# Kernel tuning notes

Measured on AMD Instinct MI355X. Metric: run time of the kernel, lower is better.

## Reference

```python
import jax, jax.numpy as jnp
import numpy as np

NUM_HEADS = 16
HEAD_DIM = 80  # head_dim_ori; NPU pads 80->128 with zeros (math-neutral)


def _rotate_half(x):
    x1, x2 = jnp.split(x, 2, axis=-1)
    return jnp.concatenate([-x2, x1], axis=-1)


def setup_inputs() -> dict:
    key = jax.random.key(0)
    ks = jax.random.split(key, 7)
    S, E = 4096, 1280
    inv = jnp.asarray(1.0 / np.sqrt(E), jnp.float32)
    # rotary tables: proper cos/sin from angles for realism
    pos = jnp.arange(S, dtype=jnp.float32)[:, None]
    freqs = 1.0 / (10000.0 ** (jnp.arange(0, HEAD_DIM // 2, dtype=jnp.float32) / (HEAD_DIM // 2)))
    ang = pos * freqs[None, :]                      # [S, 40]
    ang = jnp.concatenate([ang, ang], axis=-1)      # [S, 80] rotate-half layout
    return {
        'hidden_states': jax.random.normal(ks[0], (S, E), jnp.float32),
        'cos': jnp.cos(ang),
        'sin': jnp.sin(ang),
        'w_qkv': jax.random.normal(ks[1], (3 * E, E), jnp.float32) * inv,
        'b_qkv': jax.random.normal(ks[2], (3 * E,), jnp.float32) * 0.02,
        'w_proj': jax.random.normal(ks[3], (E, E), jnp.float32) * inv,
        'b_proj': jax.random.normal(ks[4], (E,), jnp.float32) * 0.02,
    }


def reference(hidden_states, cos, sin, w_qkv, b_qkv, w_proj, b_proj):
    S, E = hidden_states.shape
    H, D = NUM_HEADS, HEAD_DIM
    # fused QKV linear (transposeB=True, hasBias=True) then split into 3
    qkv = hidden_states @ w_qkv.T + b_qkv          # [S, 3E]
    q, k, v = jnp.split(qkv, 3, axis=-1)
    q = q.reshape(S, H, D)
    k = k.reshape(S, H, D)
    v = v.reshape(S, H, D)
    # rotate-half RoPE (rotaryCoeff=2) on q and k
    c = cos[:, None, :]
    s = sin[:, None, :]
    q = q * c + _rotate_half(q) * s
    k = k * c + _rotate_half(k) * s
    # full bidirectional self-attention (PA_ENCODER), qkScale = 1/sqrt(head_dim_ori)
    scale = jnp.asarray(1.0 / np.sqrt(D), q.dtype)
    scores = jnp.einsum('shd,thd->hst', q, k) * scale   # [H, S, S]
    attn = jax.nn.softmax(scores, axis=-1)
    out = jnp.einsum('hst,thd->shd', attn, v).reshape(S, E)
    # output projection + residual add (atten_res_add)
    dense = out @ w_proj.T + b_proj
    return hidden_states + dense
```

## Files before the change

### kernel.cpp

```cpp
#include <hip/hip_runtime.h>
#include <hip/hip_bf16.h>


#define S_LEN 4096
#define E_DIM 1280
#define NH 16
#define HD 80
#define HDP 96

typedef __bf16 bf16x8 __attribute__((ext_vector_type(8)));
typedef float f32x4 __attribute__((ext_vector_type(4)));

__device__ __forceinline__ short f2bf(float x) {
    __hip_bfloat16 h = __float2bfloat16(x);
    return __builtin_bit_cast(short, h);
}
__device__ __forceinline__ float bf2f(short x) {
    return __bfloat162float(__builtin_bit_cast(__hip_bfloat16, x));
}
__device__ __forceinline__ bf16x8 ldb(const short* p) {
    return *reinterpret_cast<const bf16x8*>(p);
}
__device__ __forceinline__ unsigned cvt_pk_bf16(float a, float b) {
    unsigned r;
    asm("v_cvt_pk_bf16_f32 %0, %1, %2" : "=v"(r) : "v"(a), "v"(b));
    return r;
}
__device__ __forceinline__ void gload16(const void* g, void* l) {
    __builtin_amdgcn_global_load_lds(
        (const __attribute__((address_space(1))) unsigned int*)g,
        (__attribute__((address_space(3))) unsigned int*)l, 16, 0, 0);
}

__global__ __launch_bounds__(256) void cast3_k(const float* __restrict__ a, short* __restrict__ oa, int na4,
                                               const float* __restrict__ b, short* __restrict__ ob, int nb4,
                                               const float* __restrict__ c, short* __restrict__ oc, int nc4) {
    int j = blockIdx.x * 256 + threadIdx.x;
    const float* src;
    short* dst;
    if (j < na4) {
        src = a; dst = oa;
    } else {
        j -= na4;
        if (j < nb4) {
            src = b; dst = ob;
        } else {
            j -= nb4;
            if (j >= nc4) return;
            src = c; dst = oc;
        }
    }
    float4 v = *reinterpret_cast<const float4*>(&src[j * 4]);
    ushort4 o;
    o.x = (unsigned short)f2bf(v.x);
    o.y = (unsigned short)f2bf(v.y);
    o.z = (unsigned short)f2bf(v.z);
    o.w = (unsigned short)f2bf(v.w);
    *reinterpret_cast<ushort4*>(&dst[j * 4]) = o;
}

__global__ __launch_bounds__(512, 2) void gemm1_256_k(
    const short* __restrict__ A, const short* __restrict__ B, const float* __restrict__ bias,
    short* __restrict__ Qraw, short* __restrict__ Kraw, short* __restrict__ Vg) {
    const int K = E_DIM;
    __shared__ short As[2][2][8192];
    __shared__ short Bs[2][2][8192];
    int t = threadIdx.x;
    int lane = t & 63, w = t >> 6;
    int wr = w >> 2, wc = w & 3;
    int lr = lane & 15, lg = lane >> 4;
    int bid = blockIdx.x;
    int swz = (bid & 7) * 30 + (bid >> 3);
    int bm = swz / 15, bn = swz % 15;
    int mb = bm * 256, nb = bn * 256;

    int lgs = (t & 3) ^ ((t >> 3) & 3);
    const short* aS = A + (size_t)(mb + (t >> 2)) * K + lgs * 8;
    const short* bS = B + (size_t)(nb + (t >> 2)) * K + lgs * 8;
    const int rowStep = 128 * K;

    int aoff[2][4], boff[4];
#pragma unroll
    for (int mq = 0; mq < 2; mq++)
#pragma unroll
        for (int ii = 0; ii < 4; ii++) {
            int r = wr * 128 + mq * 64 + ii * 16 + lr;
            aoff[mq][ii] = r * 32 + ((lg ^ ((r >> 1) & 3)) * 8);
        }
#pragma unroll
    for (int n = 0; n < 4; n++) {
        int r = wc * 64 + n * 16 + lr;
        boff[n] = r * 32 + ((lg ^ ((r >> 1) & 3)) * 8);
    }

    f32x4 acc[8][4];
#pragma unroll
    for (int i = 0; i < 8; i++)
#pragma unroll
        for (int n = 0; n < 4; n++) acc[i][n] = (f32x4){0.f, 0.f, 0.f, 0.f};

#define STG_A(d, kh, kb2)                                              \
    {                                                                  \
        gload16(aS + (kb2) + (kh)*32, &As[d][kh][w * 512]);            \
        gload16(aS + rowStep + (kb2) + (kh)*32, &As[d][kh][4096 + w * 512]); \
    }
#define STG_B(d, kh, kb2)                                              \
    {                                                                  \
        gload16(bS + (kb2) + (kh)*32, &Bs[d][kh][w * 512]);            \
        gload16(bS + rowStep + (kb2) + (kh)*32, &Bs[d][kh][4096 + w * 512]); \
    }

    STG_A(0, 0, 0);
    STG_B(0, 0, 0);
    STG_A(0, 1, 0);
    STG_B(0, 1, 0);
    asm volatile("s_waitcnt vmcnt(4)" ::: "memory");
    __builtin_amdgcn_s_barrier();
    asm volatile("" ::: "memory");

    for (int kb = 0; kb < K; kb += 64) {
        int d = (kb >> 6) & 1;
        int kb2 = kb + 64;
        bool more = kb2 < K;
        bf16x8 af[4], bfr[4];

#pragma unroll
        for (int n = 0; n < 4; n++) bfr[n] = ldb(&Bs[d][0][boff[n]]);
#pragma unroll
        for (int ii = 0; ii < 4; ii++) af[ii] = ldb(&As[d][0][aoff[0][ii]]);
        if (more) STG_A(d ^ 1, 0, kb2);
        __builtin_amdgcn_s_barrier();
        asm volatile("s_waitcnt lgkmcnt(0)" ::: "memory");
        __builtin_amdgcn_sched_barrier(0);
        __builtin_amdgcn_s_setprio(1);
#pragma unroll
        for (int ii = 0; ii < 4; ii++)
#pragma unroll
            for (int n = 0; n < 4; n++)
                acc[ii][n] = __builtin_amdgcn_mfma_f32_16x16x32_bf16(af[ii], bfr[n], acc[ii][n], 0, 0, 0);
        __builtin_amdgcn_s_setprio(0);
        __builtin_amdgcn_s_barrier();
        asm volatile("" ::: "memory");

#pragma unroll
        for (int ii = 0; ii < 4; ii++) af[ii] = ldb(&As[d][0][aoff[1][ii]]);
        if (more) {
            STG_B(d ^ 1, 0, kb2);
            asm volatile("s_waitcnt vmcnt(4)" ::: "memory");
        } else {
            asm volatile("s_waitcnt vmcnt(0)" ::: "memory");
        }
        __builtin_amdgcn_s_barrier();
        asm volatile("s_waitcnt lgkmcnt(0)" ::: "memory");
        __builtin_amdgcn_sched_barrier(0);
        __builtin_amdgcn_s_setprio(1);
#pragma unroll
        for (int ii = 0; ii < 4; ii++)
#pragma unroll
            for (int n = 0; n < 4; n++)
                acc[4 + ii][n] = __builtin_amdgcn_mfma_f32_16x16x32_bf16(af[ii], bfr[n], acc[4 + ii][n], 0, 0, 0);
        __builtin_amdgcn_s_setprio(0);
        __builtin_amdgcn_s_barrier();
        asm volatile("" ::: "memory");

#pragma unroll
        for (int n = 0; n < 4; n++) bfr[n] = ldb(&Bs[d][1][boff[n]]);
#pragma unroll
        for (int ii = 0; ii < 4; ii++) af[ii] = ldb(&As[d][1][aoff[0][ii]]);
        if (more) STG_A(d ^ 1, 1, kb2);
        __builtin_amdgcn_s_barrier();
        asm volatile("s_waitcnt lgkmcnt(0)" ::: "memory");
        __builtin_amdgcn_sched_barrier(0);
        __builtin_amdgcn_s_setprio(1);
#pragma unroll
        for (int ii = 0; ii < 4; ii++)
#pragma unroll
            for (int n = 0; n < 4; n++)
                acc[ii][n] = __builtin_amdgcn_mfma_f32_16x16x32_bf16(af[ii], bfr[n], acc[ii][n], 0, 0, 0);
        __builtin_amdgcn_s_setprio(0);
        __builtin_amdgcn_s_barrier();
        asm volatile("" ::: "memory");

#pragma unroll
        for (int ii = 0; ii < 4; ii++) af[ii] = ldb(&As[d][1][aoff[1][ii]]);
        if (more) {
            STG_B(d ^ 1, 1, kb2);
            asm volatile("s_waitcnt vmcnt(4)" ::: "memory");
        }
        __builtin_amdgcn_s_barrier();
        asm volatile("s_waitcnt lgkmcnt(0)" ::: "memory");
        __builtin_amdgcn_sched_barrier(0);
        __builtin_amdgcn_s_setprio(1);
#pragma unroll
        for (int ii = 0; ii < 4; ii++)
#pragma unroll
            for (int n = 0; n < 4; n++)
                acc[4 + ii][n] = __builtin_amdgcn_mfma_f32_16x16x32_bf16(af[ii], bfr[n], acc[4 + ii][n], 0, 0, 0);
        __builtin_amdgcn_s_setprio(0);
        __builtin_amdgcn_s_barrier();
        asm volatile("" ::: "memory");
    }
#undef STG_A
#undef STG_B

    int part = nb / E_DIM;
    short* dst = (part == 0) ? Qraw : (part == 1) ? Kraw : Vg;
    int nloc = nb - part * E_DIM;
#pragma unroll
    for (int j = 0; j < 4; j++) {
        int cn = wc * 64 + j * 16 + lr;
        float bv = bias[nb + cn];
        int col = nloc + cn;
#pragma unroll
        for (int i = 0; i < 8; i++) {
#pragma unroll
            for (int r = 0; r < 4; r++) {
                int s = mb + wr * 128 + (i >> 2) * 64 + (i & 3) * 16 + lg * 4 + r;
                dst[(size_t)s * E_DIM + col] = f2bf(acc[i][j][r] + bv);
            }
        }
    }
}

__global__ __launch_bounds__(256) void gemm_bt_k(
    const short* __restrict__ A, const short* __restrict__ B, const float* __restrict__ bias,
    const float* __restrict__ resid, float* __restrict__ Out) {
    const int K = E_DIM;
    __shared__ short As[2][128 * 64];
    __shared__ short Bs[2][128 * 64];
    int t = threadIdx.x;
    int lane = t & 63, w = t >> 6;
    int wr = w >> 1, wc = w & 1;
    int lr = lane & 15, lg = lane >> 4;
    int mb = blockIdx.y * 128, nb = blockIdx.x * 128;

    const short* asrc[4];
    const short* bsrc[4];
#pragma unroll
    for (int c = 0; c < 4; c++) {
        int p = c * 256 + t;
        int m = p >> 3;
        int kg = (p & 7) ^ (m & 7);
        asrc[c] = A + (size_t)(mb + m) * K + kg * 8;
        bsrc[c] = B + (size_t)(nb + m) * K + kg * 8;
    }
    int xa = lr & 7;
    int cx0 = ((0 * 4 + lg) ^ xa) * 8;
    int cx1 = ((1 * 4 + lg) ^ xa) * 8;
    int rowA[4], rowB[4];
#pragma unroll
    for (int i = 0; i < 4; i++) {
        rowA[i] = (wr * 64 + i * 16 + lr) * 64;
        rowB[i] = (wc * 64 + i * 16 + lr) * 64;
    }

    f32x4 acc[4][4];
#pragma unroll
    for (int i = 0; i < 4; i++)
#pragma unroll
        for (int j = 0; j < 4; j++) acc[i][j] = (f32x4){0.f, 0.f, 0.f, 0.f};

#define G_STAGE(buf, kb)                                             \
    {                                                                \
        _Pragma("unroll") for (int c = 0; c < 4; c++) {              \
            int ldso = c * 2048 + w * 512;                           \
            gload16(asrc[c] + (kb), &As[buf][ldso]);                 \
            gload16(bsrc[c] + (kb), &Bs[buf][ldso]);                 \
        }                                                            \
    }

    G_STAGE(0, 0);
    asm volatile("s_waitcnt vmcnt(0)" ::: "memory");
    __syncthreads();

    int buf = 0;
    for (int kb = 0; kb < K; kb += 64) {
        if (kb + 64 < K) G_STAGE(buf ^ 1, kb + 64);
        __builtin_amdgcn_s_setprio(1);
#pragma unroll
        for (int kk = 0; kk < 2; kk++) {
            int cx = kk ? cx1 : cx0;
            bf16x8 af[4], bfr[4];
#pragma unroll
            for (int i = 0; i < 4; i++) {
                af[i] = ldb(&As[buf][rowA[i] + cx]);
                bfr[i] = ldb(&Bs[buf][rowB[i] + cx]);
            }
#pragma unroll
            for (int i = 0; i < 4; i++)
#pragma unroll
                for (int j = 0; j < 4; j++)
                    acc[i][j] = __builtin_amdgcn_mfma_f32_16x16x32_bf16(af[i], bfr[j], acc[i][j], 0, 0, 0);
        }
        __builtin_amdgcn_s_setprio(0);
        __syncthreads();
        buf ^= 1;
    }
#undef G_STAGE

#pragma unroll
    for (int j = 0; j < 4; j++) {
        int n = nb + wc * 64 + j * 16 + lr;
        float bv = bias[n];
#pragma unroll
        for (int i = 0; i < 4; i++) {
#pragma unroll
            for (int r = 0; r < 4; r++) {
                int s = mb + wr * 64 + i * 16 + lg * 4 + r;
                Out[s * E_DIM + n] = acc[i][j][r] + bv + resid[s * E_DIM + n];
            }
        }
    }
}

__global__ __launch_bounds__(256) void rope_k(const short* __restrict__ Qraw,
                                              const short* __restrict__ Kraw,
                                              const float* __restrict__ cosp,
                                              const float* __restrict__ sinp,
                                              short* __restrict__ Qg, short* __restrict__ Kg) {
    int idx = blockIdx.x * 256 + threadIdx.x;
    int c = idx % 12;
    int hh = (idx / 12) & 15;
    int s = idx / 192;
    int base96 = ((hh * S_LEN + s)) * HDP + c * 8;
    if (c >= 10) {
        int4 z = {0, 0, 0, 0};
        *reinterpret_cast<int4*>(&Qg[base96]) = z;
        *reinterpret_cast<int4*>(&Kg[base96]) = z;
        return;
    }
    int d0 = c * 8;
    int dp = (d0 < 40) ? d0 + 40 : d0 - 40;
    float sgn = (d0 < 40) ? -1.f : 1.f;
    int base80 = s * E_DIM + hh * HD;
    float q[8], qp[8], k[8], kp[8], cs[8], sn[8];
    {
        int4 v;
        v = *reinterpret_cast<const int4*>(&Qraw[base80 + d0]);
        const short* sp = reinterpret_cast<const short*>(&v);
        for (int i = 0; i < 8; i++) q[i] = bf2f(sp[i]);
        v = *reinterpret_cast<const int4*>(&Qraw[base80 + dp]);
        for (int i = 0; i < 8; i++) qp[i] = bf2f(sp[i]);
        v = *reinterpret_cast<const int4*>(&Kraw[base80 + d0]);
        for (int i = 0; i < 8; i++) k[i] = bf2f(sp[i]);
        v = *reinterpret_cast<const int4*>(&Kraw[base80 + dp]);
        for (int i = 0; i < 8; i++) kp[i] = bf2f(sp[i]);
    }
    *reinterpret_cast<float4*>(&cs[0]) = *reinterpret_cast<const float4*>(&cosp[s * HD + d0]);
    *reinterpret_cast<float4*>(&cs[4]) = *reinterpret_cast<const float4*>(&cosp[s * HD + d0 + 4]);
    *reinterpret_cast<float4*>(&sn[0]) = *reinterpret_cast<const float4*>(&sinp[s * HD + d0]);
    *reinterpret_cast<float4*>(&sn[4]) = *reinterpret_cast<const float4*>(&sinp[s * HD + d0 + 4]);
    const float qscale = 0.16129849190f;
    short oq[8], ok[8];
#pragma unroll
    for (int i = 0; i < 8; i++) {
        oq[i] = f2bf((q[i] * cs[i] + sgn * qp[i] * sn[i]) * qscale);
        ok[i] = f2bf(k[i] * cs[i] + sgn * kp[i] * sn[i]);
    }
    *reinterpret_cast<int4*>(&Qg[base96]) = *reinterpret_cast<int4*>(oq);
    *reinterpret_cast<int4*>(&Kg[base96]) = *reinterpret_cast<int4*>(ok);
}

__global__ __launch_bounds__(256) void transpose_v_k(const short* __restrict__ Vg,
                                                     short* __restrict__ Vt) {
    __shared__ short tile[32][33];
    int h = blockIdx.z, sb = blockIdx.x * 32, db = blockIdx.y * 32;
    int t = threadIdx.x;
    for (int e = t; e < 1024; e += 256) {
        int si = e >> 5, dj = e & 31;
        int d = db + dj;
        tile[si][dj] = (d < HD) ? Vg[(size_t)(sb + si) * E_DIM + h * HD + d] : (short)0;
    }
    __syncthreads();
    for (int e = t; e < 1024; e += 256) {
        int di = e >> 5, sj = e & 31;
        int d = db + di;
        int pj = ((sj >> 2) & 3) * 8 + ((sj >> 4) & 1) * 4 + (sj & 3);
        if (d < HD) Vt[(h * HD + d) * S_LEN + sb + pj] = tile[sj][di];
    }
}

__global__ __launch_bounds__(512, 4) void attn_k(const short* __restrict__ Qg,
                                                 const short* __restrict__ Kg,
                                                 const short* __restrict__ Vt,
                                                 short* __restrict__ Ob) {
    __shared__ __align__(16) short smem[24832];
    short* ksb = smem;
    short* vsb = smem + 13312;

    int t = threadIdx.x;
    int lane = t & 63, w = t >> 6;
    int lr = lane & 15, lg = lane >> 4;
    int pairi = w >> 1, half = w & 1;
    int L = blockIdx.x;
    int h = ((L & 7) << 1) | (L >> 8);
    int qb = ((L >> 3) & 31) << 7;

    const short* kgp = Kg + (size_t)h * S_LEN * HDP;
    const short* vgp = Vt + (size_t)h * HD * S_LEN;

    bf16x8 qf[2][3];
#pragma unroll
    for (int qq = 0; qq < 2; qq++) {
        const short* qp = Qg + ((size_t)h * S_LEN + qb + pairi * 32 + qq * 16 + lr) * HDP;
#pragma unroll
        for (int kk = 0; kk < 3; kk++) qf[qq][kk] = ldb(qp + kk * 32 + lg * 8);
    }
    f32x4 o[2][5];
#pragma unroll
    for (int qq = 0; qq < 2; qq++)
#pragma unroll
        for (int nd = 0; nd < 5; nd++) o[qq][nd] = (f32x4){0.f, 0.f, 0.f, 0.f};
    f32x4 l4[2] = {(f32x4){0.f, 0.f, 0.f, 0.f}, (f32x4){0.f, 0.f, 0.f, 0.f}};

    int gk0 = t, rk0 = gk0 / 13, ok0 = gk0 % 13;
    if (ok0 == 12) ok0 = 0;
    const short* ksrc0 = kgp + rk0 * HDP + ok0 * 8;
    int gk1 = t + 512, rk1 = gk1 / 13, ok1 = gk1 % 13;
    if (ok1 == 12) ok1 = 0;
    const short* ksrc1 = kgp + rk1 * HDP + ok1 * 8;
    int gv0 = t, rv0 = gv0 / 9, ov0 = gv0 % 9;
    if (ov0 == 8) ov0 = 0;
    const short* vsrc0 = vgp + (size_t)rv0 * S_LEN + ov0 * 8;
    bool v1v = (t + 512) < 720;
    int gv1 = t + 512, rv1 = gv1 / 9, ov1 = gv1 % 9;
    if (ov1 == 8) ov1 = 0;
    const short* vsrc1 = vgp + (size_t)rv1 * S_LEN + ov1 * 8;

#define A_STAGE(buf, kb)                                                          \
    {                                                                             \
        gload16(ksrc0 + (size_t)(kb) * HDP, ksb + (buf)*6656 + w * 512);          \
        if (w < 5) gload16(ksrc1 + (size_t)(kb) * HDP, ksb + (buf)*6656 + 4096 + w * 512); \
        gload16(vsrc0 + (kb), vsb + (buf)*5760 + w * 512);                        \
        if (v1v) gload16(vsrc1 + (kb), vsb + (buf)*5760 + 4096 + w * 512);        \
    }

    A_STAGE(0, 0);
    asm volatile("s_waitcnt vmcnt(0)" ::: "memory");
    __syncthreads();

    int buf = 0;
    for (int kb = 0; kb < S_LEN; kb += 64) {
        if (kb + 64 < S_LEN) A_STAGE(buf ^ 1, kb + 64);
        const short* ks = ksb + buf * 6656;
        const short* vs = vsb + buf * 5760;

        f32x4 sc[2][2];
#pragma unroll
        for (int qq = 0; qq < 2; qq++)
#pragma unroll
            for (int n = 0; n < 2; n++) sc[qq][n] = (f32x4){0.f, 0.f, 0.f, 0.f};
        __builtin_amdgcn_s_setprio(1);
#pragma unroll
        for (int n = 0; n < 2; n++) {
#pragma unroll
            for (int kk = 0; kk < 3; kk++) {
                bf16x8 kf = ldb(&ks[(half * 32 + n * 16 + lr) * 104 + kk * 32 + lg * 8]);
                sc[0][n] = __builtin_amdgcn_mfma_f32_16x16x32_bf16(kf, qf[0][kk], sc[0][n], 0, 0, 0);
                sc[1][n] = __builtin_amdgcn_mfma_f32_16x16x32_bf16(kf, qf[1][kk], sc[1][n], 0, 0, 0);
            }
        }
        __builtin_amdgcn_s_setprio(0);

        bf16x8 pa[2];
#pragma unroll
        for (int qq = 0; qq < 2; qq++) {
#pragma unroll
            for (int n = 0; n < 2; n++) {
#pragma unroll
                for (int r = 0; r < 4; r++) sc[qq][n][r] = __builtin_amdgcn_exp2f(sc[qq][n][r]);
                l4[qq] += sc[qq][n];
            }
            uint4 pw;
            pw.x = cvt_pk_bf16(sc[qq][0][0], sc[qq][0][1]);
            pw.y = cvt_pk_bf16(sc[qq][0][2], sc[qq][0][3]);
            pw.z = cvt_pk_bf16(sc[qq][1][0], sc[qq][1][1]);
            pw.w = cvt_pk_bf16(sc[qq][1][2], sc[qq][1][3]);
            pa[qq] = __builtin_bit_cast(bf16x8, pw);
        }

        __builtin_amdgcn_s_setprio(1);
#pragma unroll
        for (int nd = 0; nd < 5; nd++) {
            bf16x8 vf = ldb(&vs[(nd * 16 + lr) * 72 + half * 32 + lg * 8]);
            o[0][nd] = __builtin_amdgcn_mfma_f32_16x16x32_bf16(pa[0], vf, o[0][nd], 0, 0, 0);
            o[1][nd] = __builtin_amdgcn_mfma_f32_16x16x32_bf16(pa[1], vf, o[1][nd], 0, 0, 0);
        }
        __builtin_amdgcn_s_setprio(0);

        __syncthreads();
        buf ^= 1;
    }
#undef A_STAGE

    float lh[2];
#pragma unroll
    for (int qq = 0; qq < 2; qq++) {
        float l = l4[qq][0] + l4[qq][1] + l4[qq][2] + l4[qq][3];
        l += __shfl_xor(l, 16);
        l += __shfl_xor(l, 32);
        lh[qq] = l;
    }
    float* Osc = reinterpret_cast<float*>(smem);
    float* lsc = reinterpret_cast<float*>(smem) + 10240;
    if (half) {
#pragma unroll
        for (int qq = 0; qq < 2; qq++) {
#pragma unroll
            for (int nd = 0; nd < 5; nd++)
#pragma unroll
                for (int r = 0; r < 4; r++)
                    Osc[(pairi * 32 + qq * 16 + lg * 4 + r) * 80 + nd * 16 + lr] = o[qq][nd][r];
            if (lg == 0) lsc[pairi * 32 + qq * 16 + lr] = lh[qq];
        }
    }
    __syncthreads();
    if (!half) {
        float rl[2][4];
#pragma unroll
        for (int qq = 0; qq < 2; qq++) {
            float lt = lh[qq] + lsc[pairi * 32 + qq * 16 + lr];
#pragma unroll
            for (int r = 0; r < 4; r++) {
                float lf = __shfl(lt, lg * 4 + r);
                rl[qq][r] = __builtin_amdgcn_rcpf(lf);
            }
        }
#pragma unroll
        for (int qq = 0; qq < 2; qq++)
#pragma unroll
            for (int nd = 0; nd < 5; nd++)
#pragma unroll
                for (int r = 0; r < 4; r++) {
                    int s = qb + pairi * 32 + qq * 16 + lg * 4 + r;
                    float val = o[qq][nd][r] + Osc[(pairi * 32 + qq * 16 + lg * 4 + r) * 80 + nd * 16 + lr];
                    Ob[s * E_DIM + h * HD + nd * 16 + lr] = f2bf(val * rl[qq][r]);
                }
    }
}

extern "C" void kernel_launch(void* const* d_in, const int* in_sizes, int n_in,
                              void* d_out, int out_size, void* d_ws, size_t ws_size,
                              hipStream_t stream) {
    const float* hidden = (const float*)d_in[0];
    const float* cosp = (const float*)d_in[1];
    const float* sinp = (const float*)d_in[2];
    const float* wqkv = (const float*)d_in[3];
    const float* bqkv = (const float*)d_in[4];
    const float* wproj = (const float*)d_in[5];
    const float* bproj = (const float*)d_in[6];
    float* out = (float*)d_out;

    char* p = (char*)d_ws;
    short* Xb = (short*)p;      p += (size_t)S_LEN * E_DIM * 2;
    short* Wqkvb = (short*)p;   p += (size_t)3 * E_DIM * E_DIM * 2;
    short* Wprojb = (short*)p;  p += (size_t)E_DIM * E_DIM * 2;
    short* Qraw = (short*)p;    p += (size_t)S_LEN * E_DIM * 2;
    short* Kraw = (short*)p;    p += (size_t)S_LEN * E_DIM * 2;
    short* Vg = (short*)p;      p += (size_t)S_LEN * E_DIM * 2;
    short* Qg = (short*)p;      p += (size_t)NH * S_LEN * HDP * 2;
    short* Kg = (short*)p;      p += (size_t)NH * S_LEN * HDP * 2;
    short* Vt = (short*)p;      p += (size_t)NH * HD * S_LEN * 2;
    short* Ob = Xb;

    const int na4 = S_LEN * E_DIM / 4;
    const int nb4 = 3 * E_DIM * E_DIM / 4;
    const int nc4 = E_DIM * E_DIM / 4;
    cast3_k<<<(na4 + nb4 + nc4 + 255) / 256, 256, 0, stream>>>(
        hidden, Xb, na4, wqkv, Wqkvb, nb4, wproj, Wprojb, nc4);

    gemm1_256_k<<<dim3(240), 512, 0, stream>>>(Xb, Wqkvb, bqkv, Qraw, Kraw, Vg);

    rope_k<<<S_LEN * 192 / 256, 256, 0, stream>>>(Qraw, Kraw, cosp, sinp, Qg, Kg);

    transpose_v_k<<<dim3(S_LEN / 32, 3, NH), 256, 0, stream>>>(Vg, Vt);

    attn_k<<<dim3(512), 512, 0, stream>>>(Qg, Kg, Vt, Ob);

    gemm_bt_k<<<dim3(E_DIM / 128, S_LEN / 128), 256, 0, stream>>>(
        Ob, Wprojb, bproj, hidden, out);
}
```

Measured before the change: 197.3 us.

## Fuse RoPE into QKV GEMM epilogue via interleaved weight-row permutation

While casting the QKV weights to bf16, the Q and K rows of each head are permuted so that each rotate-half partner pair sits in adjacent columns. The GEMM epilogue then applies bias, RoPE (partner value fetched with a lane xor-1 shuffle) and the Q scale. It writes straight into the padded per-head Q/K layout and zero-fills the padding. This removes the separate rope kernel and the Qraw/Kraw intermediate round trip through global memory. In exchange the epilogue does per-element cos/sin loads and shuffles, and the head dimension of Q and K is stored permuted, which is harmless because both use the same permutation in the dot product.

Result: slower. 209.2 us (+6.0%).

```diff
diff --git a/kernel.cpp b/kernel.cpp
--- a/kernel.cpp
+++ b/kernel.cpp
@@ -14,9 +14,6 @@
 __device__ __forceinline__ short f2bf(float x) {
     __hip_bfloat16 h = __float2bfloat16(x);
     return __builtin_bit_cast(short, h);
-}
-__device__ __forceinline__ float bf2f(short x) {
-    return __bfloat162float(__builtin_bit_cast(__hip_bfloat16, x));
 }
 __device__ __forceinline__ bf16x8 ldb(const short* p) {
     return *reinterpret_cast<const bf16x8*>(p);
@@ -38,12 +35,13 @@
     int j = blockIdx.x * 256 + threadIdx.x;
     const float* src;
     short* dst;
+    bool remap = false;
     if (j < na4) {
         src = a; dst = oa;
     } else {
         j -= na4;
         if (j < nb4) {
-            src = b; dst = ob;
+            src = b; dst = ob; remap = true;
         } else {
             j -= nb4;
             if (j >= nc4) return;
@@ -51,17 +49,29 @@
         }
     }
     float4 v = *reinterpret_cast<const float4*>(&src[j * 4]);
+    int dj = j;
+    if (remap) {
+        int row = j / 320, c4 = j - row * 320;
+        if (row < 2560) {
+            int part = row / 1280;
+            int loc = row - part * 1280;
+            int hh = loc / 80, d = loc - hh * 80;
+            int dp = (d < 40) ? 2 * d : 2 * (d - 40) + 1;
+            dj = (part * 1280 + hh * 80 + dp) * 320 + c4;
+        }
+    }
     ushort4 o;
     o.x = (unsigned short)f2bf(v.x);
     o.y = (unsigned short)f2bf(v.y);
     o.z = (unsigned short)f2bf(v.z);
     o.w = (unsigned short)f2bf(v.w);
-    *reinterpret_cast<ushort4*>(&dst[j * 4]) = o;
+    *reinterpret_cast<ushort4*>(&dst[dj * 4]) = o;
 }
 
 __global__ __launch_bounds__(512, 2) void gemm1_256_k(
     const short* __restrict__ A, const short* __restrict__ B, const float* __restrict__ bias,
-    short* __restrict__ Qraw, short* __restrict__ Kraw, short* __restrict__ Vg) {
+    const float* __restrict__ cosp, const float* __restrict__ sinp,
+    short* __restrict__ Qg, short* __restrict__ Kg, short* __restrict__ Vg) {
     const int K = E_DIM;
     __shared__ short As[2][2][8192];
     __shared__ short Bs[2][2][8192];
@@ -204,19 +214,48 @@
 #undef STG_B
 
     int part = nb / E_DIM;
-    short* dst = (part == 0) ? Qraw : (part == 1) ? Kraw : Vg;
-    int nloc = nb - part * E_DIM;
-#pragma unroll
-    for (int j = 0; j < 4; j++) {
-        int cn = wc * 64 + j * 16 + lr;
-        float bv = bias[nb + cn];
-        int col = nloc + cn;
-#pragma unroll
-        for (int i = 0; i < 8; i++) {
-#pragma unroll
-            for (int r = 0; r < 4; r++) {
-                int s = mb + wr * 128 + (i >> 2) * 64 + (i & 3) * 16 + lg * 4 + r;
-                dst[(size_t)s * E_DIM + col] = f2bf(acc[i][j][r] + bv);
+    if (part < 2) {
+        short* dst = part ? Kg : Qg;
+        const float scl = part ? 1.0f : 0.16129849190f;
+#pragma unroll
+        for (int j = 0; j < 4; j++) {
+            int cn = wc * 64 + j * 16 + lr;
+            int pcol = nb - part * E_DIM + cn;
+            int hh = pcol / 80;
+            int dl = pcol - hh * 80;
+            int i2 = dl >> 1;
+            int parity = dl & 1;
+            float bv = bias[part * E_DIM + hh * 80 + (parity ? i2 + 40 : i2)];
+            size_t hbase = (size_t)hh * S_LEN * HDP;
+#pragma unroll
+            for (int i = 0; i < 8; i++) {
+#pragma unroll
+                for (int r = 0; r < 4; r++) {
+                    int s = mb + wr * 128 + (i >> 2) * 64 + (i & 3) * 16 + lg * 4 + r;
+                    float v = acc[i][j][r] + bv;
+                    float pv = __shfl_xor(v, 1);
+                    float cc = cosp[s * HD + i2];
+                    float ss = sinp[s * HD + i2];
+                    float ov = fmaf(v, cc, parity ? pv * ss : -pv * ss) * scl;
+                    size_t rowb = hbase + (size_t)s * HDP;
+                    dst[rowb + dl] = f2bf(ov);
+                    if (dl >= 64) dst[rowb + dl + 16] = 0;
+                }
+            }
+        }
+    } else {
+#pragma unroll
+        for (int j = 0; j < 4; j++) {
+            int cn = wc * 64 + j * 16 + lr;
+            float bv = bias[nb + cn];
+            int col = nb - 2 * E_DIM + cn;
+#pragma unroll
+            for (int i = 0; i < 8; i++) {
+#pragma unroll
+                for (int r = 0; r < 4; r++) {
+                    int s = mb + wr * 128 + (i >> 2) * 64 + (i & 3) * 16 + lg * 4 + r;
+                    Vg[(size_t)s * E_DIM + col] = f2bf(acc[i][j][r] + bv);
+                }
             }
         }
     }
@@ -311,54 +350,6 @@
             }
         }
     }
-}
-
-__global__ __launch_bounds__(256) void rope_k(const short* __restrict__ Qraw,
-                                              const short* __restrict__ Kraw,
-                                              const float* __restrict__ cosp,
-                                              const float* __restrict__ sinp,
-                                              short* __restrict__ Qg, short* __restrict__ Kg) {
-    int idx = blockIdx.x * 256 + threadIdx.x;
-    int c = idx % 12;
-    int hh = (idx / 12) & 15;
-    int s = idx / 192;
-    int base96 = ((hh * S_LEN + s)) * HDP + c * 8;
-    if (c >= 10) {
-        int4 z = {0, 0, 0, 0};
-        *reinterpret_cast<int4*>(&Qg[base96]) = z;
-        *reinterpret_cast<int4*>(&Kg[base96]) = z;
-        return;
-    }
-    int d0 = c * 8;
-    int dp = (d0 < 40) ? d0 + 40 : d0 - 40;
-    float sgn = (d0 < 40) ? -1.f : 1.f;
-    int base80 = s * E_DIM + hh * HD;
-    float q[8], qp[8], k[8], kp[8], cs[8], sn[8];
-    {
-        int4 v;
-        v = *reinterpret_cast<const int4*>(&Qraw[base80 + d0]);
-        const short* sp = reinterpret_cast<const short*>(&v);
-        for (int i = 0; i < 8; i++) q[i] = bf2f(sp[i]);
-        v = *reinterpret_cast<const int4*>(&Qraw[base80 + dp]);
-        for (int i = 0; i < 8; i++) qp[i] = bf2f(sp[i]);
-        v = *reinterpret_cast<const int4*>(&Kraw[base80 + d0]);
-        for (int i = 0; i < 8; i++) k[i] = bf2f(sp[i]);
-        v = *reinterpret_cast<const int4*>(&Kraw[base80 + dp]);
-        for (int i = 0; i < 8; i++) kp[i] = bf2f(sp[i]);
-    }
-    *reinterpret_cast<float4*>(&cs[0]) = *reinterpret_cast<const float4*>(&cosp[s * HD + d0]);
-    *reinterpret_cast<float4*>(&cs[4]) = *reinterpret_cast<const float4*>(&cosp[s * HD + d0 + 4]);
-    *reinterpret_cast<float4*>(&sn[0]) = *reinterpret_cast<const float4*>(&sinp[s * HD + d0]);
-    *reinterpret_cast<float4*>(&sn[4]) = *reinterpret_cast<const float4*>(&sinp[s * HD + d0 + 4]);
-    const float qscale = 0.16129849190f;
-    short oq[8], ok[8];
-#pragma unroll
-    for (int i = 0; i < 8; i++) {
-        oq[i] = f2bf((q[i] * cs[i] + sgn * qp[i] * sn[i]) * qscale);
-        ok[i] = f2bf(k[i] * cs[i] + sgn * kp[i] * sn[i]);
-    }
-    *reinterpret_cast<int4*>(&Qg[base96]) = *reinterpret_cast<int4*>(oq);
-    *reinterpret_cast<int4*>(&Kg[base96]) = *reinterpret_cast<int4*>(ok);
 }
 
 __global__ __launch_bounds__(256) void transpose_v_k(const short* __restrict__ Vg,
@@ -555,8 +546,6 @@
     short* Xb = (short*)p;      p += (size_t)S_LEN * E_DIM * 2;
     short* Wqkvb = (short*)p;   p += (size_t)3 * E_DIM * E_DIM * 2;
     short* Wprojb = (short*)p;  p += (size_t)E_DIM * E_DIM * 2;
-    short* Qraw = (short*)p;    p += (size_t)S_LEN * E_DIM * 2;
-    short* Kraw = (short*)p;    p += (size_t)S_LEN * E_DIM * 2;
     short* Vg = (short*)p;      p += (size_t)S_LEN * E_DIM * 2;
     short* Qg = (short*)p;      p += (size_t)NH * S_LEN * HDP * 2;
     short* Kg = (short*)p;      p += (size_t)NH * S_LEN * HDP * 2;
@@ -569,9 +558,7 @@
     cast3_k<<<(na4 + nb4 + nc4 + 255) / 256, 256, 0, stream>>>(
         hidden, Xb, na4, wqkv, Wqkvb, nb4, wproj, Wprojb, nc4);
 
-    gemm1_256_k<<<dim3(240), 512, 0, stream>>>(Xb, Wqkvb, bqkv, Qraw, Kraw, Vg);
-
-    rope_k<<<S_LEN * 192 / 256, 256, 0, stream>>>(Qraw, Kraw, cosp, sinp, Qg, Kg);
+    gemm1_256_k<<<dim3(240), 512, 0, stream>>>(Xb, Wqkvb, bqkv, cosp, sinp, Qg, Kg, Vg);
 
     transpose_v_k<<<dim3(S_LEN / 32, 3, NH), 256, 0, stream>>>(Vg, Vt);
 
```
